# Kernel tuning notes

Hardware: AMD Instinct MI355X
Metric: run time of the kernel (lower is better)

## Reference

```python
import jax, jax.numpy as jnp
import numpy as np

N_NODES = 100000
N_EDGES = 1600000
N_GRAPHS = 4096
EPS = 1e-5


def setup_inputs() -> dict:
    key = jax.random.key(0)
    ks = jax.random.split(key, 12)
    x = jax.random.normal(ks[0], (N_NODES, 9), dtype=jnp.float32)
    edge_index = jax.random.randint(ks[1], (2, N_EDGES), 0, N_NODES, dtype=jnp.int64)
    batch = jnp.sort(jax.random.randint(ks[2], (N_NODES,), 0, N_GRAPHS, dtype=jnp.int64))
    w0 = jax.random.normal(ks[3], (9, 128), dtype=jnp.float32) * 0.3
    w12 = jax.random.normal(ks[4], (2, 128, 128), dtype=jnp.float32) * 0.09
    cb = jax.random.normal(ks[5], (3, 128), dtype=jnp.float32) * 0.02
    bn_g = jnp.ones((3, 128), dtype=jnp.float32)
    bn_b = jnp.zeros((3, 128), dtype=jnp.float32)
    m0w = jax.random.normal(ks[6], (256, 256), dtype=jnp.float32) * 0.06
    m0b = jnp.zeros((256,), dtype=jnp.float32)
    m1w = jax.random.normal(ks[7], (256, 64), dtype=jnp.float32) * 0.06
    m1b = jnp.zeros((64,), dtype=jnp.float32)
    m2w = jax.random.normal(ks[8], (64, 1), dtype=jnp.float32) * 0.12
    m2b = jnp.zeros((1,), dtype=jnp.float32)
    return {"x": x, "edge_index": edge_index, "batch": batch, "w0": w0, "w12": w12,
            "cb": cb, "bn_g": bn_g, "bn_b": bn_b, "m0w": m0w, "m0b": m0b,
            "m1w": m1w, "m1b": m1b, "m2w": m2w, "m2b": m2b}


def reference(x, edge_index, batch, w0, w12, cb, bn_g, bn_b, m0w, m0b, m1w, m1b, m2w, m2b):
    N = x.shape[0]
    loops = jnp.arange(N, dtype=edge_index.dtype)
    src = jnp.concatenate([edge_index[0], loops])  # [E+N]
    dst = jnp.concatenate([edge_index[1], loops])
    # symmetric GCN normalization with self-loops: deg^-1/2 on both ends
    deg = jax.ops.segment_sum(jnp.ones(src.shape, dtype=x.dtype), dst, num_segments=N)
    dinv = jax.lax.rsqrt(jnp.maximum(deg, 1.0))
    enorm = (dinv[src] * dinv[dst])[:, None]  # [E+N, 1]

    def gcn_bn_relu(h, W, b, g, beta):
        h = h @ W                                            # [N, H]
        agg = jax.ops.segment_sum(h[src] * enorm, dst, num_segments=N) + b
        mu = agg.mean(axis=0)
        var = agg.var(axis=0)  # biased, as in BatchNorm training forward
        hn = (agg - mu) * jax.lax.rsqrt(var + EPS) * g + beta
        return jax.nn.relu(hn)

    h = gcn_bn_relu(x, w0, cb[0], bn_g[0], bn_b[0])
    h = gcn_bn_relu(h, w12[0], cb[1], bn_g[1], bn_b[1])
    h = gcn_bn_relu(h, w12[1], cb[2], bn_g[2], bn_b[2])

    # global mean / max pool over graphs
    cnt = jax.ops.segment_sum(jnp.ones((N,), dtype=h.dtype), batch, num_segments=N_GRAPHS)
    xs = jax.ops.segment_sum(h, batch, num_segments=N_GRAPHS)
    x_mean = xs / jnp.maximum(cnt, 1.0)[:, None]
    x_max = jax.ops.segment_max(h, batch, num_segments=N_GRAPHS)
    x_max = jnp.where(jnp.isfinite(x_max), x_max, 0.0)
    xg = jnp.concatenate([x_mean, x_max], axis=1)  # [G, 256]

    hm = jax.nn.relu(xg @ m0w + m0b)
    hm = jax.nn.relu(hm @ m1w + m1b)
    out = hm @ m2w + m2b
    return out[:, 0]
```

## Files before the change

kernel.cpp:

```cpp
#include <hip/hip_runtime.h>

#define NN 100000
#define NE 1600000
#define NG 4096
#define HD 128
#define EPSV 1e-5f
#define NBUCK 391
#define BIN_CHUNK 4096
#define NBIN_BLK ((NE + BIN_CHUNK - 1) / BIN_CHUNK)
#define CSR_CAP 8448
#define NB_AG 4096
#define CH_AG 25
#define NB_MM 2048
#define CH_MM 49

typedef _Float16 half_t;
typedef _Float16 half8 __attribute__((ext_vector_type(8)));
typedef _Float16 half4v __attribute__((ext_vector_type(4)));
typedef _Float16 half2v __attribute__((ext_vector_type(2)));
typedef float f32x4 __attribute__((ext_vector_type(4)));


__global__ void k_zero_i32(int* p, int n) {
    int i = blockIdx.x * blockDim.x + threadIdx.x;
    if (i < n) p[i] = 0;
}

__global__ void k_bcount(const int* __restrict__ ei, int* __restrict__ bcnt) {
    __shared__ int cnt[NBUCK];
    int t = threadIdx.x;
    for (int i = t; i < NBUCK; i += 256) cnt[i] = 0;
    __syncthreads();
    int e0 = blockIdx.x * BIN_CHUNK;
    int e1 = min(NE, e0 + BIN_CHUNK);
    for (int e = e0 + t; e < e1; e += 256)
        atomicAdd(&cnt[ei[NE + e] >> 8], 1);
    __syncthreads();
    for (int i = t; i < NBUCK; i += 256)
        if (cnt[i]) atomicAdd(&bcnt[i], cnt[i]);
}

__global__ void k_bscan(const int* __restrict__ bcnt, int* __restrict__ ebase, int* __restrict__ gcur) {
    __shared__ int s[512];
    int t = threadIdx.x;
    int v = (t < NBUCK) ? bcnt[t] : 0;
    s[t] = v;
    __syncthreads();
    for (int off = 1; off < 512; off <<= 1) {
        int x = (t >= off) ? s[t - off] : 0;
        __syncthreads();
        s[t] += x;
        __syncthreads();
    }
    if (t <= NBUCK) {
        int ex = s[t] - v;
        ebase[t] = ex;
        if (t < NBUCK) gcur[t] = ex;
    }
}

__global__ void k_bin(const int* __restrict__ ei, int* __restrict__ gcur, unsigned* __restrict__ binned) {
    __shared__ int cnt[NBUCK];
    __shared__ int cur[NBUCK];
    int t = threadIdx.x;
    for (int i = t; i < NBUCK; i += 256) cnt[i] = 0;
    __syncthreads();
    int e0 = blockIdx.x * BIN_CHUNK;
    int e1 = min(NE, e0 + BIN_CHUNK);
    for (int e = e0 + t; e < e1; e += 256)
        atomicAdd(&cnt[ei[NE + e] >> 8], 1);
    __syncthreads();
    for (int i = t; i < NBUCK; i += 256)
        cur[i] = cnt[i] ? atomicAdd(&gcur[i], cnt[i]) : 0;
    __syncthreads();
    for (int e = e0 + t; e < e1; e += 256) {
        int d = ei[NE + e];
        int b = d >> 8;
        int r = atomicAdd(&cur[b], 1);
        binned[r] = ((unsigned)ei[e] << 8) | (unsigned)(d & 255);
    }
}

__global__ __launch_bounds__(256) void k_csr(const unsigned* __restrict__ binned,
        const int* __restrict__ ebase, int* __restrict__ rp,
        float* __restrict__ dinv, int* __restrict__ col) {
    __shared__ int colb[CSR_CAP];
    __shared__ int deg[256], off[256], cur[256], s[256];
    int b = blockIdx.x, t = threadIdx.x;
    int n0 = b * 256;
    int nodes = min(256, NN - n0);
    int cbeg = ebase[b];
    int cnt_b = min(ebase[b + 1] - cbeg, CSR_CAP - 256);
    int base = cbeg + n0;
    deg[t] = 0;
    __syncthreads();
    for (int i = t; i < cnt_b; i += 256)
        atomicAdd(&deg[binned[cbeg + i] & 255], 1);
    __syncthreads();
    int w = (t < nodes) ? deg[t] + 1 : 0;
    s[t] = w;
    __syncthreads();
    for (int o = 1; o < 256; o <<= 1) {
        int x = (t >= o) ? s[t - o] : 0;
        __syncthreads();
        s[t] += x;
        __syncthreads();
    }
    int ex = s[t] - w;
    off[t] = ex;
    cur[t] = ex;
    if (t < nodes) {
        rp[n0 + t] = base + ex;
        dinv[n0 + t] = rsqrtf((float)(deg[t] + 1));
    }
    __syncthreads();
    for (int i = t; i < cnt_b; i += 256) {
        unsigned pk = binned[cbeg + i];
        int d = pk & 255;
        int r = atomicAdd(&cur[d], 1);
        colb[r] = (int)(pk >> 8);
    }
    __syncthreads();
    if (t < nodes) colb[cur[t]] = n0 + t;
    __syncthreads();
    int tot = cnt_b + nodes;
    for (int i = t; i < tot; i += 256) col[base + i] = colb[i];
    if (b == 0 && t == 0) rp[NN] = NE + NN;
}


__global__ void k_cvtw(const float* __restrict__ w12, half_t* __restrict__ Wt) {
    int i = blockIdx.x * 256 + threadIdx.x;
    int m = i >> 14;
    int r = i & 16383;
    int n = r >> 7, k = r & 127;
    Wt[i] = (half_t)w12[m * 16384 + k * 128 + n];
}


__global__ void k_padx(const float* __restrict__ x, const float* __restrict__ dinv,
                       half_t* __restrict__ xh) {
    int n = blockIdx.x * 256 + threadIdx.x;
    if (n >= NN) return;
    float dv = dinv[n];
    half_t buf[16];
#pragma unroll
    for (int k = 0; k < 9; ++k) buf[k] = (half_t)(x[n * 9 + k] * dv);
#pragma unroll
    for (int k = 9; k < 16; ++k) buf[k] = (half_t)0.f;
    *(half8*)&xh[n * 16] = *(half8*)buf;
    *(half8*)&xh[n * 16 + 8] = *(half8*)(buf + 8);
}

__global__ void k_aggx(const half_t* __restrict__ xh, const float* __restrict__ dinv,
                       float* __restrict__ aggx,
                       const int* __restrict__ rp, const int* __restrict__ col) {
    int t = blockIdx.x * blockDim.x + threadIdx.x;
    int n = t >> 2, sub = (t & 3) * 4;
    if (n >= NN) return;
    int s = rp[n], e = rp[n + 1];
    float acc[4] = {0.f, 0.f, 0.f, 0.f};
    int i = s;
    for (; i + 1 < e; i += 2) {
        half4v v0 = *(const half4v*)&xh[col[i] * 16 + sub];
        half4v v1 = *(const half4v*)&xh[col[i + 1] * 16 + sub];
#pragma unroll
        for (int j = 0; j < 4; ++j) acc[j] += (float)v0[j] + (float)v1[j];
    }
    if (i < e) {
        half4v v0 = *(const half4v*)&xh[col[i] * 16 + sub];
#pragma unroll
        for (int j = 0; j < 4; ++j) acc[j] += (float)v0[j];
    }
    float dv = dinv[n];
    f32x4 o = {acc[0] * dv, acc[1] * dv, acc[2] * dv, acc[3] * dv};
    *(f32x4*)&aggx[n * 16 + sub] = o;
}

__global__ __launch_bounds__(256) void k_mm9(const float* __restrict__ aggx,
        const float* __restrict__ w0, half_t* __restrict__ gout,
        float* __restrict__ ps, float* __restrict__ ps2) {
    __shared__ float lsum[4][128], lsq[4][128];
    int t = threadIdx.x, w = t >> 6, l = t & 63;
    int c = 2 * l;
    int n0 = blockIdx.x * CH_MM;
    int n1 = min(NN, n0 + CH_MM);
    float s0 = 0.f, s1 = 0.f, q0 = 0.f, q1 = 0.f;
    for (int n = n0 + w; n < n1; n += 4) {
        float2 acc = make_float2(0.f, 0.f);
#pragma unroll
        for (int k = 0; k < 9; ++k) {
            float a = aggx[n * 16 + k];
            float2 wv = *(const float2*)&w0[k * HD + c];
            acc.x += a * wv.x;
            acc.y += a * wv.y;
        }
        half_t hx = (half_t)acc.x, hy = (half_t)acc.y;
        half2v hv = {hx, hy};
        *(half2v*)&gout[n * HD + c] = hv;
        float fx = (float)hx, fy = (float)hy;
        s0 += fx; q0 += fx * fx; s1 += fy; q1 += fy * fy;
    }
    lsum[w][c] = s0; lsum[w][c + 1] = s1;
    lsq[w][c] = q0;  lsq[w][c + 1] = q1;
    __syncthreads();
    if (t < 128) {
        ps[blockIdx.x * 128 + t] = lsum[0][t] + lsum[1][t] + lsum[2][t] + lsum[3][t];
        ps2[blockIdx.x * 128 + t] = lsq[0][t] + lsq[1][t] + lsq[2][t] + lsq[3][t];
    }
}

__global__ __launch_bounds__(256) void k_stats2(const float* __restrict__ ps,
        const float* __restrict__ ps2, const float* __restrict__ g,
        const float* __restrict__ be, float* __restrict__ scale,
        float* __restrict__ shift, int nb) {
    __shared__ float sa[256], sb[256];
    int c = blockIdx.x, t = threadIdx.x;
    float S = 0.f, Q = 0.f;
    for (int i = t; i < nb; i += 256) {
        S += ps[i * 128 + c];
        Q += ps2[i * 128 + c];
    }
    sa[t] = S; sb[t] = Q;
    __syncthreads();
    for (int o = 128; o; o >>= 1) {
        if (t < o) { sa[t] += sa[t + o]; sb[t] += sb[t + o]; }
        __syncthreads();
    }
    if (t == 0) {
        double mu = (double)sa[0] / NN;
        double var = (double)sb[0] / NN - mu * mu;
        float sc = g[c] * rsqrtf((float)var + EPSV);
        scale[c] = sc;
        shift[c] = be[c] - (float)mu * sc;
    }
}


__global__ __launch_bounds__(256) void k_mm_mfma(const half_t* __restrict__ gf,
        const float* __restrict__ scale, const float* __restrict__ shift,
        const float* __restrict__ dinv, const half_t* __restrict__ Wt,
        half_t* __restrict__ hh) {
    __shared__ half_t wlds[16384];
    int t = threadIdx.x;
#pragma unroll
    for (int j = 0; j < 8; ++j) {
        int cidx = t * 8 + j;
        int n = cidx >> 4, k8 = cidx & 15;
        half8 v = *(const half8*)&Wt[cidx * 8];
        int byte = n * 256 + ((k8 * 16) ^ ((n & 7) << 4));
        *(half8*)((char*)wlds + byte) = v;
    }
    __syncthreads();
    int w = t >> 6, l = t & 63;
    int lr = l & 15, lg = l >> 4;
    int base = (blockIdx.x * 4 + w) * 16;
    int row = base + lr;
    bool rowok = row < NN;
    f32x4 acc[8];
#pragma unroll
    for (int nt = 0; nt < 8; ++nt) acc[nt] = (f32x4){0.f, 0.f, 0.f, 0.f};
#pragma unroll
    for (int kk = 0; kk < 4; ++kk) {
        int ch0 = kk * 32 + lg * 8;
        half8 a8;
        if (rowok) {
            half8 hv = *(const half8*)&gf[row * HD + ch0];
            f32x4 sc0 = *(const f32x4*)&scale[ch0];
            f32x4 sc1 = *(const f32x4*)&scale[ch0 + 4];
            f32x4 sh0 = *(const f32x4*)&shift[ch0];
            f32x4 sh1 = *(const f32x4*)&shift[ch0 + 4];
#pragma unroll
            for (int i = 0; i < 4; ++i)
                a8[i] = (half_t)fmaxf((float)hv[i] * sc0[i] + sh0[i], 0.f);
#pragma unroll
            for (int i = 0; i < 4; ++i)
                a8[4 + i] = (half_t)fmaxf((float)hv[4 + i] * sc1[i] + sh1[i], 0.f);
        } else {
#pragma unroll
            for (int i = 0; i < 8; ++i) a8[i] = (half_t)0.f;
        }
        int kbyte = kk * 64 + lg * 16;
#pragma unroll
        for (int nt = 0; nt < 8; ++nt) {
            int n = nt * 16 + lr;
            half8 b8 = *(const half8*)((const char*)wlds + n * 256 + (kbyte ^ ((n & 7) << 4)));
            acc[nt] = __builtin_amdgcn_mfma_f32_16x16x32_f16(a8, b8, acc[nt], 0, 0, 0);
        }
    }
#pragma unroll
    for (int i = 0; i < 4; ++i) {
        int r = base + lg * 4 + i;
        if (r < NN) {
            float dv = dinv[r];
#pragma unroll
            for (int nt = 0; nt < 8; ++nt)
                hh[r * HD + nt * 16 + lr] = (half_t)(acc[nt][i] * dv);
        }
    }
}


__global__ __launch_bounds__(256) void k_agg_h(const half_t* __restrict__ hh,
        const float* __restrict__ dinv, half_t* __restrict__ gout,
        const int* __restrict__ rp, const int* __restrict__ col,
        float* __restrict__ ps, float* __restrict__ ps2) {
    __shared__ float lsum[16][128], lsq[16][128];
    int t = threadIdx.x, w = t >> 6, l = t & 63;
    int sub = l >> 4, li = l & 15;
    int sg = w * 4 + sub;
    int c0 = li * 8;
    int n0 = blockIdx.x * CH_AG;
    int n1 = min(NN, n0 + CH_AG);
    float sacc[8], qacc[8];
#pragma unroll
    for (int j = 0; j < 8; ++j) { sacc[j] = 0.f; qacc[j] = 0.f; }
    for (int n = n0 + sg; n < n1; n += 16) {
        int s = rp[n], e = rp[n + 1];
        float facc[8];
#pragma unroll
        for (int j = 0; j < 8; ++j) facc[j] = 0.f;
        int i = s;
        for (; i + 1 < e; i += 2) {
            int ca = col[i], cb = col[i + 1];
            half8 v0 = *(const half8*)&hh[ca * HD + c0];
            half8 v1 = *(const half8*)&hh[cb * HD + c0];
#pragma unroll
            for (int j = 0; j < 8; ++j) facc[j] += (float)v0[j] + (float)v1[j];
        }
        if (i < e) {
            half8 v0 = *(const half8*)&hh[col[i] * HD + c0];
#pragma unroll
            for (int j = 0; j < 8; ++j) facc[j] += (float)v0[j];
        }
        float dv = dinv[n];
        half8 hv;
#pragma unroll
        for (int j = 0; j < 8; ++j) hv[j] = (half_t)(facc[j] * dv);
        *(half8*)&gout[n * HD + c0] = hv;
#pragma unroll
        for (int j = 0; j < 8; ++j) {
            float f = (float)hv[j];
            sacc[j] += f;
            qacc[j] += f * f;
        }
    }
#pragma unroll
    for (int j = 0; j < 8; ++j) {
        lsum[sg][c0 + j] = sacc[j];
        lsq[sg][c0 + j] = qacc[j];
    }
    __syncthreads();
    if (t < 128) {
        float S = 0.f, Q = 0.f;
#pragma unroll
        for (int g = 0; g < 16; ++g) { S += lsum[g][t]; Q += lsq[g][t]; }
        ps[blockIdx.x * 128 + t] = S;
        ps2[blockIdx.x * 128 + t] = Q;
    }
}


__global__ void k_pool_fused(const half_t* __restrict__ h, const float* __restrict__ scale,
                             const float* __restrict__ shift, const int* __restrict__ batch,
                             float* __restrict__ xg) {
    int l = threadIdx.x & 63;
    int g = blockIdx.x * (blockDim.x >> 6) + (threadIdx.x >> 6);
    if (g >= NG) return;
    int c = 2 * l;
    float2 sc = make_float2(scale[c], scale[c + 1]);
    float2 sh = make_float2(shift[c], shift[c + 1]);
    int lo = 0, hi = NN;
    while (lo < hi) { int m = (lo + hi) >> 1; if (batch[m] < g) lo = m + 1; else hi = m; }
    int s = lo;
    hi = NN;
    while (lo < hi) { int m = (lo + hi) >> 1; if (batch[m] < g + 1) lo = m + 1; else hi = m; }
    int e = lo;
    float2 sum = make_float2(0.f, 0.f), mx = make_float2(-3e38f, -3e38f);
    for (int r = s; r < e; ++r) {
        half2v hv = *(const half2v*)&h[r * HD + c];
        float vx = fmaxf((float)hv[0] * sc.x + sh.x, 0.f);
        float vy = fmaxf((float)hv[1] * sc.y + sh.y, 0.f);
        sum.x += vx; sum.y += vy;
        mx.x = fmaxf(mx.x, vx); mx.y = fmaxf(mx.y, vy);
    }
    float2 mean = make_float2(0.f, 0.f), mxo = make_float2(0.f, 0.f);
    if (e > s) {
        float cnt = (float)(e - s);
        mean.x = sum.x / cnt; mean.y = sum.y / cnt;
        mxo = mx;
    }
    *(float2*)&xg[g * 256 + c] = mean;
    *(float2*)&xg[g * 256 + 128 + c] = mxo;
}

#define GPB 8
__global__ __launch_bounds__(256) void k_mlp(const float* __restrict__ xg,
                                             const float* __restrict__ m0w, const float* __restrict__ m0b,
                                             const float* __restrict__ m1w, const float* __restrict__ m1b,
                                             const float* __restrict__ m2w, const float* __restrict__ m2b,
                                             float* __restrict__ out) {
    __shared__ float xs[GPB][256];
    __shared__ float h1[GPB][256];
    __shared__ float h2[GPB][64];
    int t = threadIdx.x;
    int g0 = blockIdx.x * GPB;
#pragma unroll
    for (int j = 0; j < GPB; ++j) xs[j][t] = xg[(g0 + j) * 256 + t];
    __syncthreads();
    float acc[GPB];
#pragma unroll
    for (int j = 0; j < GPB; ++j) acc[j] = m0b[t];
    for (int i = 0; i < 256; ++i) {
        float wv = m0w[i * 256 + t];
#pragma unroll
        for (int j = 0; j < GPB; ++j) acc[j] += xs[j][i] * wv;
    }
#pragma unroll
    for (int j = 0; j < GPB; ++j) h1[j][t] = fmaxf(acc[j], 0.f);
    __syncthreads();
    if (t < 64) {
        float a2[GPB];
#pragma unroll
        for (int j = 0; j < GPB; ++j) a2[j] = m1b[t];
        for (int i = 0; i < 256; ++i) {
            float wv = m1w[i * 64 + t];
#pragma unroll
            for (int j = 0; j < GPB; ++j) a2[j] += h1[j][i] * wv;
        }
#pragma unroll
        for (int j = 0; j < GPB; ++j) h2[j][t] = fmaxf(a2[j], 0.f);
    }
    __syncthreads();
    if (t < 64) {
#pragma unroll
        for (int j = 0; j < GPB; ++j) {
            float v = h2[j][t] * m2w[t];
            for (int off = 32; off; off >>= 1) v += __shfl_down(v, off);
            if (t == 0) out[g0 + j] = v + m2b[0];
        }
    }
}


extern "C" void kernel_launch(void* const* d_in, const int* in_sizes, int n_in,
                              void* d_out, int out_size, void* d_ws, size_t ws_size,
                              hipStream_t stream) {
    const float* x    = (const float*)d_in[0];
    const int*   ei   = (const int*)d_in[1];
    const int*   batch= (const int*)d_in[2];
    const float* w0   = (const float*)d_in[3];
    const float* w12  = (const float*)d_in[4];
    const float* bn_g = (const float*)d_in[6];
    const float* bn_b = (const float*)d_in[7];
    const float* m0w  = (const float*)d_in[8];
    const float* m0b  = (const float*)d_in[9];
    const float* m1w  = (const float*)d_in[10];
    const float* m1b  = (const float*)d_in[11];
    const float* m2w  = (const float*)d_in[12];
    const float* m2b  = (const float*)d_in[13];
    float* out = (float*)d_out;

    char* p = (char*)d_ws;
    auto alloc = [&](size_t bytes) {
        void* r = (void*)p;
        p += (bytes + 255) & ~(size_t)255;
        return r;
    };
    half_t*   gf0    = (half_t*)alloc((size_t)NN * HD * 2);
    half_t*   gf1    = (half_t*)alloc((size_t)NN * HD * 2);
    half_t*   hh     = (half_t*)alloc((size_t)NN * HD * 2);
    half_t*   xh     = (half_t*)alloc((size_t)NN * 16 * 2);
    float*    aggx   = (float*)alloc((size_t)NN * 16 * 4);
    half_t*   Wt     = (half_t*)alloc((size_t)2 * 128 * 128 * 2);
    float*    dinv   = (float*)alloc((size_t)NN * 4);
    int*      rp     = (int*)alloc((size_t)(NN + 1) * 4);
    int*      col    = (int*)alloc((size_t)(NE + NN) * 4);
    unsigned* binned = (unsigned*)alloc((size_t)NE * 4);
    int*      bcnt   = (int*)alloc(512 * 4);
    int*      ebase  = (int*)alloc(512 * 4);
    int*      gcur   = (int*)alloc(512 * 4);
    float*    ps     = (float*)alloc((size_t)NB_AG * 128 * 4);
    float*    ps2    = (float*)alloc((size_t)NB_AG * 128 * 4);
    float*    scb    = (float*)alloc(3 * 128 * 4);
    float*    shb    = (float*)alloc(3 * 128 * 4);
    float*    xg     = (float*)alloc((size_t)NG * 256 * 4);

    k_zero_i32<<<2, 256, 0, stream>>>(bcnt, 512);
    k_bcount<<<NBIN_BLK, 256, 0, stream>>>(ei, bcnt);
    k_bscan<<<1, 512, 0, stream>>>(bcnt, ebase, gcur);
    k_bin<<<NBIN_BLK, 256, 0, stream>>>(ei, gcur, binned);
    k_csr<<<NBUCK, 256, 0, stream>>>(binned, ebase, rp, dinv, col);

    k_cvtw<<<128, 256, 0, stream>>>(w12, Wt);

    k_padx<<<(NN + 255) / 256, 256, 0, stream>>>(x, dinv, xh);
    k_aggx<<<(NN * 4 + 255) / 256, 256, 0, stream>>>(xh, dinv, aggx, rp, col);
    k_mm9<<<NB_MM, 256, 0, stream>>>(aggx, w0, gf0, ps, ps2);
    k_stats2<<<128, 256, 0, stream>>>(ps, ps2, bn_g + 0, bn_b + 0, scb + 0, shb + 0, NB_MM);

    k_mm_mfma<<<(NN + 63) / 64, 256, 0, stream>>>(gf0, scb + 0, shb + 0, dinv, Wt, hh);
    k_agg_h<<<NB_AG, 256, 0, stream>>>(hh, dinv, gf1, rp, col, ps, ps2);
    k_stats2<<<128, 256, 0, stream>>>(ps, ps2, bn_g + 128, bn_b + 128, scb + 128, shb + 128, NB_AG);

    k_mm_mfma<<<(NN + 63) / 64, 256, 0, stream>>>(gf1, scb + 128, shb + 128, dinv, Wt + 16384, hh);
    k_agg_h<<<NB_AG, 256, 0, stream>>>(hh, dinv, gf0, rp, col, ps, ps2);
    k_stats2<<<128, 256, 0, stream>>>(ps, ps2, bn_g + 256, bn_b + 256, scb + 256, shb + 256, NB_AG);

    k_pool_fused<<<NG / 4, 256, 0, stream>>>(gf0, scb + 256, shb + 256, batch, xg);
    k_mlp<<<NG / GPB, 256, 0, stream>>>(xg, m0w, m0b, m1w, m1b, m2w, m2b, out);
}
```

Baseline: 368.4 us.

## Merge prep kernels, store aggx in fp16, fuse pooling into MLP kernel

Combines the weight-transpose and input-padding kernels into one launch, stores the first-layer aggregated features as fp16 instead of fp32, and fuses global mean/max pooling directly into the MLP kernel so pooled features stay in shared memory. Also drops an unused shared array in the CSR kernel. This is meant to cut launch overhead and global-memory traffic. In exchange it adds an extra fp16 rounding of the aggregated inputs. The pooling now uses 512 blocks instead of 1024, with each wave handling two graphs serially, which lowers parallelism in that phase.

```diff
diff --git a/kernel.cpp b/kernel.cpp
--- a/kernel.cpp
+++ b/kernel.cpp
@@ -85,7 +85,7 @@
         const int* __restrict__ ebase, int* __restrict__ rp,
         float* __restrict__ dinv, int* __restrict__ col) {
     __shared__ int colb[CSR_CAP];
-    __shared__ int deg[256], off[256], cur[256], s[256];
+    __shared__ int deg[256], cur[256], s[256];
     int b = blockIdx.x, t = threadIdx.x;
     int n0 = b * 256;
     int nodes = min(256, NN - n0);
@@ -107,7 +107,6 @@
         __syncthreads();
     }
     int ex = s[t] - w;
-    off[t] = ex;
     cur[t] = ex;
     if (t < nodes) {
         rp[n0 + t] = base + ex;
@@ -129,31 +128,33 @@
 }
 
 
-__global__ void k_cvtw(const float* __restrict__ w12, half_t* __restrict__ Wt) {
-    int i = blockIdx.x * 256 + threadIdx.x;
-    int m = i >> 14;
-    int r = i & 16383;
-    int n = r >> 7, k = r & 127;
-    Wt[i] = (half_t)w12[m * 16384 + k * 128 + n];
-}
-
-
-__global__ void k_padx(const float* __restrict__ x, const float* __restrict__ dinv,
+__global__ void k_prep(const float* __restrict__ w12, half_t* __restrict__ Wt,
+                       const float* __restrict__ x, const float* __restrict__ dinv,
                        half_t* __restrict__ xh) {
-    int n = blockIdx.x * 256 + threadIdx.x;
-    if (n >= NN) return;
-    float dv = dinv[n];
-    half_t buf[16];
-#pragma unroll
-    for (int k = 0; k < 9; ++k) buf[k] = (half_t)(x[n * 9 + k] * dv);
-#pragma unroll
-    for (int k = 9; k < 16; ++k) buf[k] = (half_t)0.f;
-    *(half8*)&xh[n * 16] = *(half8*)buf;
-    *(half8*)&xh[n * 16 + 8] = *(half8*)(buf + 8);
-}
+    int b = blockIdx.x;
+    if (b < 128) {
+        int i = b * 256 + threadIdx.x;
+        int m = i >> 14;
+        int r = i & 16383;
+        int n = r >> 7, k = r & 127;
+        Wt[i] = (half_t)w12[m * 16384 + k * 128 + n];
+    } else {
+        int n = (b - 128) * 256 + threadIdx.x;
+        if (n >= NN) return;
+        float dv = dinv[n];
+        half_t buf[16];
+#pragma unroll
+        for (int k = 0; k < 9; ++k) buf[k] = (half_t)(x[n * 9 + k] * dv);
+#pragma unroll
+        for (int k = 9; k < 16; ++k) buf[k] = (half_t)0.f;
+        *(half8*)&xh[n * 16] = *(half8*)buf;
+        *(half8*)&xh[n * 16 + 8] = *(half8*)(buf + 8);
+    }
+}
+
 
 __global__ void k_aggx(const half_t* __restrict__ xh, const float* __restrict__ dinv,
-                       float* __restrict__ aggx,
+                       half_t* __restrict__ aggx,
                        const int* __restrict__ rp, const int* __restrict__ col) {
     int t = blockIdx.x * blockDim.x + threadIdx.x;
     int n = t >> 2, sub = (t & 3) * 4;
@@ -173,11 +174,12 @@
         for (int j = 0; j < 4; ++j) acc[j] += (float)v0[j];
     }
     float dv = dinv[n];
-    f32x4 o = {acc[0] * dv, acc[1] * dv, acc[2] * dv, acc[3] * dv};
-    *(f32x4*)&aggx[n * 16 + sub] = o;
-}
-
-__global__ __launch_bounds__(256) void k_mm9(const float* __restrict__ aggx,
+    half4v o = {(half_t)(acc[0] * dv), (half_t)(acc[1] * dv),
+                (half_t)(acc[2] * dv), (half_t)(acc[3] * dv)};
+    *(half4v*)&aggx[n * 16 + sub] = o;
+}
+
+__global__ __launch_bounds__(256) void k_mm9(const half_t* __restrict__ aggx,
         const float* __restrict__ w0, half_t* __restrict__ gout,
         float* __restrict__ ps, float* __restrict__ ps2) {
     __shared__ float lsum[4][128], lsq[4][128];
@@ -190,7 +192,7 @@
         float2 acc = make_float2(0.f, 0.f);
 #pragma unroll
         for (int k = 0; k < 9; ++k) {
-            float a = aggx[n * 16 + k];
+            float a = (float)aggx[n * 16 + k];
             float2 wv = *(const float2*)&w0[k * HD + c];
             acc.x += a * wv.x;
             acc.y += a * wv.y;
@@ -361,52 +363,49 @@
 }
 
 
-__global__ void k_pool_fused(const half_t* __restrict__ h, const float* __restrict__ scale,
-                             const float* __restrict__ shift, const int* __restrict__ batch,
-                             float* __restrict__ xg) {
-    int l = threadIdx.x & 63;
-    int g = blockIdx.x * (blockDim.x >> 6) + (threadIdx.x >> 6);
-    if (g >= NG) return;
-    int c = 2 * l;
-    float2 sc = make_float2(scale[c], scale[c + 1]);
-    float2 sh = make_float2(shift[c], shift[c + 1]);
-    int lo = 0, hi = NN;
-    while (lo < hi) { int m = (lo + hi) >> 1; if (batch[m] < g) lo = m + 1; else hi = m; }
-    int s = lo;
-    hi = NN;
-    while (lo < hi) { int m = (lo + hi) >> 1; if (batch[m] < g + 1) lo = m + 1; else hi = m; }
-    int e = lo;
-    float2 sum = make_float2(0.f, 0.f), mx = make_float2(-3e38f, -3e38f);
-    for (int r = s; r < e; ++r) {
-        half2v hv = *(const half2v*)&h[r * HD + c];
-        float vx = fmaxf((float)hv[0] * sc.x + sh.x, 0.f);
-        float vy = fmaxf((float)hv[1] * sc.y + sh.y, 0.f);
-        sum.x += vx; sum.y += vy;
-        mx.x = fmaxf(mx.x, vx); mx.y = fmaxf(mx.y, vy);
-    }
-    float2 mean = make_float2(0.f, 0.f), mxo = make_float2(0.f, 0.f);
-    if (e > s) {
-        float cnt = (float)(e - s);
-        mean.x = sum.x / cnt; mean.y = sum.y / cnt;
-        mxo = mx;
-    }
-    *(float2*)&xg[g * 256 + c] = mean;
-    *(float2*)&xg[g * 256 + 128 + c] = mxo;
-}
-
 #define GPB 8
-__global__ __launch_bounds__(256) void k_mlp(const float* __restrict__ xg,
-                                             const float* __restrict__ m0w, const float* __restrict__ m0b,
-                                             const float* __restrict__ m1w, const float* __restrict__ m1b,
-                                             const float* __restrict__ m2w, const float* __restrict__ m2b,
-                                             float* __restrict__ out) {
+__global__ __launch_bounds__(256) void k_poolmlp(const half_t* __restrict__ h,
+        const float* __restrict__ scale, const float* __restrict__ shift,
+        const int* __restrict__ batch,
+        const float* __restrict__ m0w, const float* __restrict__ m0b,
+        const float* __restrict__ m1w, const float* __restrict__ m1b,
+        const float* __restrict__ m2w, const float* __restrict__ m2b,
+        float* __restrict__ out) {
     __shared__ float xs[GPB][256];
     __shared__ float h1[GPB][256];
     __shared__ float h2[GPB][64];
-    int t = threadIdx.x;
+    int t = threadIdx.x, w = t >> 6, l = t & 63;
     int g0 = blockIdx.x * GPB;
-#pragma unroll
-    for (int j = 0; j < GPB; ++j) xs[j][t] = xg[(g0 + j) * 256 + t];
+    int c = 2 * l;
+    float2 sc2 = make_float2(scale[c], scale[c + 1]);
+    float2 sh2 = make_float2(shift[c], shift[c + 1]);
+#pragma unroll
+    for (int rep = 0; rep < 2; ++rep) {
+        int j = w * 2 + rep;
+        int g = g0 + j;
+        int lo = 0, hi = NN;
+        while (lo < hi) { int m = (lo + hi) >> 1; if (batch[m] < g) lo = m + 1; else hi = m; }
+        int s = lo;
+        hi = NN;
+        while (lo < hi) { int m = (lo + hi) >> 1; if (batch[m] < g + 1) lo = m + 1; else hi = m; }
+        int e = lo;
+        float2 sum = make_float2(0.f, 0.f), mx = make_float2(-3e38f, -3e38f);
+        for (int r = s; r < e; ++r) {
+            half2v hv = *(const half2v*)&h[r * HD + c];
+            float vx = fmaxf((float)hv[0] * sc2.x + sh2.x, 0.f);
+            float vy = fmaxf((float)hv[1] * sc2.y + sh2.y, 0.f);
+            sum.x += vx; sum.y += vy;
+            mx.x = fmaxf(mx.x, vx); mx.y = fmaxf(mx.y, vy);
+        }
+        float2 mean = make_float2(0.f, 0.f), mxo = make_float2(0.f, 0.f);
+        if (e > s) {
+            float cnt = (float)(e - s);
+            mean.x = sum.x / cnt; mean.y = sum.y / cnt;
+            mxo = mx;
+        }
+        xs[j][c] = mean.x; xs[j][c + 1] = mean.y;
+        xs[j][128 + c] = mxo.x; xs[j][128 + c + 1] = mxo.y;
+    }
     __syncthreads();
     float acc[GPB];
 #pragma unroll
@@ -471,7 +470,7 @@
     half_t*   gf1    = (half_t*)alloc((size_t)NN * HD * 2);
     half_t*   hh     = (half_t*)alloc((size_t)NN * HD * 2);
     half_t*   xh     = (half_t*)alloc((size_t)NN * 16 * 2);
-    float*    aggx   = (float*)alloc((size_t)NN * 16 * 4);
+    half_t*   aggx   = (half_t*)alloc((size_t)NN * 16 * 2);
     half_t*   Wt     = (half_t*)alloc((size_t)2 * 128 * 128 * 2);
     float*    dinv   = (float*)alloc((size_t)NN * 4);
     int*      rp     = (int*)alloc((size_t)(NN + 1) * 4);
@@ -484,7 +483,6 @@
     float*    ps2    = (float*)alloc((size_t)NB_AG * 128 * 4);
     float*    scb    = (float*)alloc(3 * 128 * 4);
     float*    shb    = (float*)alloc(3 * 128 * 4);
-    float*    xg     = (float*)alloc((size_t)NG * 256 * 4);
 
     k_zero_i32<<<2, 256, 0, stream>>>(bcnt, 512);
     k_bcount<<<NBIN_BLK, 256, 0, stream>>>(ei, bcnt);
@@ -492,9 +490,8 @@
     k_bin<<<NBIN_BLK, 256, 0, stream>>>(ei, gcur, binned);
     k_csr<<<NBUCK, 256, 0, stream>>>(binned, ebase, rp, dinv, col);
 
-    k_cvtw<<<128, 256, 0, stream>>>(w12, Wt);
-
-    k_padx<<<(NN + 255) / 256, 256, 0, stream>>>(x, dinv, xh);
+    k_prep<<<128 + (NN + 255) / 256, 256, 0, stream>>>(w12, Wt, x, dinv, xh);
+
     k_aggx<<<(NN * 4 + 255) / 256, 256, 0, stream>>>(xh, dinv, aggx, rp, col);
     k_mm9<<<NB_MM, 256, 0, stream>>>(aggx, w0, gf0, ps, ps2);
     k_stats2<<<128, 256, 0, stream>>>(ps, ps2, bn_g + 0, bn_b + 0, scb + 0, shb + 0, NB_MM);
@@ -507,6 +504,6 @@
     k_agg_h<<<NB_AG, 256, 0, stream>>>(hh, dinv, gf0, rp, col, ps, ps2);
     k_stats2<<<128, 256, 0, stream>>>(ps, ps2, bn_g + 256, bn_b + 256, scb + 256, shb + 256, NB_AG);
 
-    k_pool_fused<<<NG / 4, 256, 0, stream>>>(gf0, scb + 256, shb + 256, batch, xg);
-    k_mlp<<<NG / GPB, 256, 0, stream>>>(xg, m0w, m0b, m1w, m1b, m2w, m2b, out);
-}
+    k_poolmlp<<<NG / GPB, 256, 0, stream>>>(gf0, scb + 256, shb + 256, batch,
+                                            m0w, m0b, m1w, m1b, m2w, m2b, out);
+}
```

New measurement: 371.5 us. About the same (+0.8%).
